# Kernel tuning notes

Measured on AMD Instinct MI355X. Metric: run time of the kernel, lower is better.

Reference implementation:

```python
import jax, jax.numpy as jnp
import numpy as np

BS, T, H = 4, 2048, 512
N_HEAD = 8
D_HEAD = H // N_HEAD  # 64


def setup_inputs() -> dict:
    key = jax.random.key(0)
    k1, k2, k3 = jax.random.split(key, 3)
    x = jax.random.normal(k1, (BS, T, H), dtype=jnp.float32)
    # torch Linear(hidden, (2*n_head+1)*d_head) -> store transposed for x @ W
    w_qkv = jax.random.normal(k2, (H, (2 * N_HEAD + 1) * D_HEAD), dtype=jnp.float32) * (H ** -0.5)
    w_out = jax.random.normal(k3, (D_HEAD, H), dtype=jnp.float32) * (D_HEAD ** -0.5)
    return {"x": x, "w_qkv": w_qkv, "w_out": w_out}


def reference(x, w_qkv, w_out):
    bs, t, h = x.shape
    n_head, d_head = N_HEAD, D_HEAD
    scale = d_head ** -0.5

    qkv = x @ w_qkv  # [bs, t, (2*n_head+1)*d_head]
    q, k, v = jnp.split(qkv, [n_head * d_head, 2 * n_head * d_head], axis=-1)
    q = q.reshape(bs, t, n_head, d_head)
    k = k.reshape(bs, t, n_head, d_head)
    # v stays [bs, t, d_head]: a single V shared across all heads

    # causal mask: -inf strictly above the diagonal
    mask = jnp.triu(jnp.full((t, t), -jnp.inf, dtype=x.dtype), 1)

    # scores: [bs, n_head, t_q, t_k]
    attn_score = jnp.einsum('bqhd,bkhd->bhqk', q, k) * scale + mask
    attn_prob = jax.nn.softmax(attn_score, axis=-1)

    # shared V broadcast over heads: [bs, n_head, t, d_head]
    attn_vec = jnp.einsum('bhqk,bkd->bhqd', attn_prob, v)
    m_attn_vec = jnp.mean(attn_vec, axis=1)  # mean over heads -> [bs, t, d_head]

    out = m_attn_vec @ w_out  # [bs, t, hidden]
    return out, attn_prob
```

## Files before the change

kernel.cpp:

```cpp
#include <hip/hip_runtime.h>

typedef unsigned short u16;
typedef __bf16 bf16x8 __attribute__((ext_vector_type(8)));
typedef float f32x4 __attribute__((ext_vector_type(4)));
static_assert(sizeof(bf16x8) == 16, "bf16x8 must be 16B");

#define MFMA(a, b, c) __builtin_amdgcn_mfma_f32_16x16x32_bf16(a, b, c, 0, 0, 0)

__device__ __forceinline__ u16 f2bf(float f) {
  unsigned u = __float_as_uint(f);
  u += 0x7fffu + ((u >> 16) & 1u);
  return (u16)(u >> 16);
}

__global__ __launch_bounds__(256) void prep_kernel(
    const float* __restrict__ x, const float* __restrict__ wqkv,
    const float* __restrict__ wout, u16* __restrict__ xh,
    u16* __restrict__ wt, u16* __restrict__ wot) {
  int blk = blockIdx.x, tid = threadIdx.x;
  if (blk < 4096) {
    int idx = (blk * 256 + tid) * 4;
    float4 v = *(const float4*)(x + idx);
    ushort4 o;
    o.x = f2bf(v.x); o.y = f2bf(v.y); o.z = f2bf(v.z); o.w = f2bf(v.w);
    *(ushort4*)(xh + idx) = o;
  } else if (blk < 4096 + 2176) {
    int idx = (blk - 4096) * 256 + tid;
    int n = idx >> 9, k = idx & 511;
    float v = wqkv[k * 1088 + n];
    if (n < 512) v *= 0.125f;
    wt[idx] = f2bf(v);
  } else {
    int idx = (blk - 6272) * 256 + tid;
    int n = idx >> 6, d = idx & 63;
    wot[idx] = f2bf(wout[d * 512 + n]);
  }
}

__global__ __launch_bounds__(256) void qkv_gemm_kernel(
    const u16* __restrict__ xh, const u16* __restrict__ wt,
    u16* __restrict__ Qb, u16* __restrict__ Kb, u16* __restrict__ Vt) {
  __shared__ u16 As[128][40];
  __shared__ u16 Bs[64][40];
  const int tid = threadIdx.x;
  const int w = tid >> 6, l = tid & 63, g = l >> 4, c16 = l & 15;
  const int n0 = blockIdx.x * 64;
  const int m0 = blockIdx.y * 128;
  const int arow = tid >> 1, acol = (tid & 1) << 4;
  const int brow = tid >> 2, bcol = (tid & 3) << 3;
  const u16* ap = xh + (size_t)(m0 + arow) * 512 + acol;
  const u16* bp = wt + (size_t)(n0 + brow) * 512 + bcol;
  uint4 pa0 = *(const uint4*)(ap);
  uint4 pa1 = *(const uint4*)(ap + 8);
  uint4 pb0 = *(const uint4*)(bp);
  f32x4 acc[2][4] = {};
  for (int k0 = 0; k0 < 512; k0 += 32) {
    __syncthreads();
    *(uint4*)&As[arow][acol] = pa0;
    *(uint4*)&As[arow][acol + 8] = pa1;
    *(uint4*)&Bs[brow][bcol] = pb0;
    __syncthreads();
    if (k0 + 32 < 512) {
      pa0 = *(const uint4*)(ap + k0 + 32);
      pa1 = *(const uint4*)(ap + k0 + 40);
      pb0 = *(const uint4*)(bp + k0 + 32);
    }
#pragma unroll
    for (int mt = 0; mt < 2; ++mt) {
      bf16x8 a = *(const bf16x8*)&As[w * 32 + mt * 16 + c16][g * 8];
#pragma unroll
      for (int nt = 0; nt < 4; ++nt) {
        bf16x8 b = *(const bf16x8*)&Bs[nt * 16 + c16][g * 8];
        acc[mt][nt] = MFMA(a, b, acc[mt][nt]);
      }
    }
  }
#pragma unroll
  for (int mt = 0; mt < 2; ++mt)
#pragma unroll
    for (int nt = 0; nt < 4; ++nt)
#pragma unroll
      for (int j = 0; j < 4; ++j) {
        u16 bv = f2bf(acc[mt][nt][j]);
        int row = m0 + w * 32 + mt * 16 + g * 4 + j;
        int b = row >> 11, t = row & 2047;
        int col = n0 + nt * 16 + c16;
        if (col < 512) {
          int h = col >> 6, d = col & 63;
          Qb[((size_t)((b << 3) + h) * 2048 + t) * 64 + d] = bv;
        } else if (col < 1024) {
          int cc = col - 512, h = cc >> 6, d = cc & 63;
          Kb[((size_t)((b << 3) + h) * 2048 + t) * 64 + d] = bv;
        } else {
          int d = col - 1024;
          Vt[((size_t)((b << 6) + d)) * 2048 + t] = bv;
        }
      }
}

__global__ __launch_bounds__(256) void attn_kernel(
    const u16* __restrict__ Qb, const u16* __restrict__ Kb,
    const u16* __restrict__ Vt, float* __restrict__ P,
    float* __restrict__ Obuf) {
  __shared__ u16 QP[64][72];
  __shared__ u16 Ks[64][72];
  __shared__ u16 Vs[64][72];
  const int tid = threadIdx.x;
  const int w = tid >> 6, l = tid & 63, g = l >> 4, c16 = l & 15;
  const int bidx = blockIdx.x;
  const int ii = bidx >> 5, jj = bidx & 31;
  const int qt = ((ii >> 3) & 1) ? (31 - jj) : jj;
  const int bh = ii, b = bh >> 3;
  const int srow = tid >> 2, scol = (tid & 3) << 4;

  {
    const u16* src = Qb + ((size_t)(bh * 2048 + qt * 64 + srow)) * 64 + scol;
    *(uint4*)&QP[srow][scol] = *(const uint4*)(src);
    *(uint4*)&QP[srow][scol + 8] = *(const uint4*)(src + 8);
  }
  __syncthreads();
  const bf16x8 aq0 = *(const bf16x8*)&QP[w * 16 + c16][g * 8];
  const bf16x8 aq1 = *(const bf16x8*)&QP[w * 16 + c16][32 + g * 8];

  const u16* kbase = Kb + ((size_t)bh * 2048) * 64;
  const u16* vbase = Vt + ((size_t)(b << 6)) * 2048;

  float lsum = 0.f;

  uint4 ka0 = *(const uint4*)(kbase + (size_t)srow * 64 + scol);
  uint4 ka1 = *(const uint4*)(kbase + (size_t)srow * 64 + scol + 8);
  for (int kt = 0; kt <= qt; ++kt) {
    __syncthreads();
    *(uint4*)&Ks[srow][scol] = ka0;
    *(uint4*)&Ks[srow][scol + 8] = ka1;
    __syncthreads();
    if (kt < qt) {
      const u16* knext = kbase + (size_t)((kt + 1) * 64 + srow) * 64 + scol;
      ka0 = *(const uint4*)(knext);
      ka1 = *(const uint4*)(knext + 8);
    }
    f32x4 st[4];
    __builtin_amdgcn_s_setprio(1);
#pragma unroll
    for (int nt = 0; nt < 4; ++nt) {
      bf16x8 k0 = *(const bf16x8*)&Ks[nt * 16 + c16][g * 8];
      bf16x8 k1 = *(const bf16x8*)&Ks[nt * 16 + c16][32 + g * 8];
      f32x4 a = {};
      a = MFMA(k0, aq0, a);
      a = MFMA(k1, aq1, a);
      st[nt] = a;
    }
    __builtin_amdgcn_s_setprio(0);
    if (kt == qt) {
#pragma unroll
      for (int nt = 0; nt < 4; ++nt)
#pragma unroll
        for (int j = 0; j < 4; ++j)
          if (nt * 16 + g * 4 + j > w * 16 + c16) st[nt][j] = -3.0e38f;
    }
#pragma unroll
    for (int nt = 0; nt < 4; ++nt)
#pragma unroll
      for (int j = 0; j < 4; ++j) lsum += __expf(st[nt][j]);
  }
  lsum += __shfl_xor(lsum, 16, 64);
  lsum += __shfl_xor(lsum, 32, 64);
  const float rl = 1.0f / lsum;

  f32x4 oacc[4] = {};
  ka0 = *(const uint4*)(kbase + (size_t)srow * 64 + scol);
  ka1 = *(const uint4*)(kbase + (size_t)srow * 64 + scol + 8);
  uint4 va0 = *(const uint4*)(vbase + (size_t)srow * 2048 + scol);
  uint4 va1 = *(const uint4*)(vbase + (size_t)srow * 2048 + scol + 8);
  float* prow = P +
      ((size_t)(bh * 2048 + qt * 64 + w * 16 + c16)) * 2048 + g * 4;
  for (int kt = 0; kt <= qt; ++kt) {
    __syncthreads();
    *(uint4*)&Ks[srow][scol] = ka0;
    *(uint4*)&Ks[srow][scol + 8] = ka1;
    *(uint4*)&Vs[srow][scol] = va0;
    *(uint4*)&Vs[srow][scol + 8] = va1;
    __syncthreads();
    if (kt < qt) {
      const u16* knext = kbase + (size_t)((kt + 1) * 64 + srow) * 64 + scol;
      ka0 = *(const uint4*)(knext);
      ka1 = *(const uint4*)(knext + 8);
      const u16* vnext = vbase + (size_t)srow * 2048 + (kt + 1) * 64 + scol;
      va0 = *(const uint4*)(vnext);
      va1 = *(const uint4*)(vnext + 8);
    }
    f32x4 st[4];
    __builtin_amdgcn_s_setprio(1);
#pragma unroll
    for (int nt = 0; nt < 4; ++nt) {
      bf16x8 k0 = *(const bf16x8*)&Ks[nt * 16 + c16][g * 8];
      bf16x8 k1 = *(const bf16x8*)&Ks[nt * 16 + c16][32 + g * 8];
      f32x4 a = {};
      a = MFMA(k0, aq0, a);
      a = MFMA(k1, aq1, a);
      st[nt] = a;
    }
    __builtin_amdgcn_s_setprio(0);
    if (kt == qt) {
#pragma unroll
      for (int nt = 0; nt < 4; ++nt)
#pragma unroll
        for (int j = 0; j < 4; ++j)
          if (nt * 16 + g * 4 + j > w * 16 + c16) st[nt][j] = -3.0e38f;
    }
#pragma unroll
    for (int nt = 0; nt < 4; ++nt) {
      f32x4 pv;
#pragma unroll
      for (int j = 0; j < 4; ++j) pv[j] = __expf(st[nt][j]) * rl;
      __builtin_nontemporal_store(
          pv, (f32x4*)(prow + (size_t)kt * 64 + nt * 16));
      unsigned r0, r1;
      asm("v_cvt_pk_bf16_f32 %0, %1, %2" : "=v"(r0) : "v"(pv[0]), "v"(pv[1]));
      asm("v_cvt_pk_bf16_f32 %0, %1, %2" : "=v"(r1) : "v"(pv[2]), "v"(pv[3]));
      uint2 pk; pk.x = r0; pk.y = r1;
      *(uint2*)&QP[w * 16 + c16][nt * 16 + g * 4] = pk;
    }
    bf16x8 ap0 = *(const bf16x8*)&QP[w * 16 + c16][g * 8];
    bf16x8 ap1 = *(const bf16x8*)&QP[w * 16 + c16][32 + g * 8];
    __builtin_amdgcn_s_setprio(1);
#pragma unroll
    for (int nt = 0; nt < 4; ++nt) {
      bf16x8 bv0 = *(const bf16x8*)&Vs[nt * 16 + c16][g * 8];
      bf16x8 bv1 = *(const bf16x8*)&Vs[nt * 16 + c16][32 + g * 8];
      oacc[nt] = MFMA(ap0, bv0, oacc[nt]);
      oacc[nt] = MFMA(ap1, bv1, oacc[nt]);
    }
    __builtin_amdgcn_s_setprio(0);
  }

  {
    float* obase = Obuf + ((size_t)(bh * 2048 + qt * 64 + w * 16)) * 64;
#pragma unroll
    for (int nt = 0; nt < 4; ++nt)
#pragma unroll
      for (int j = 0; j < 4; ++j)
        obase[(g * 4 + j) * 64 + nt * 16 + c16] = oacc[nt][j];
  }
  {
    int colstart = (qt + 1) * 64;
    int nf4 = (2048 - colstart) >> 2;
    float* base = P + ((size_t)(bh * 2048 + qt * 64)) * 2048;
    f32x4 z = {0.f, 0.f, 0.f, 0.f};
    for (int r = 0; r < 64; ++r) {
      f32x4* rowp = (f32x4*)(base + (size_t)r * 2048 + colstart);
      for (int u = tid; u < nf4; u += 256)
        __builtin_nontemporal_store(z, rowp + u);
    }
  }
}

__global__ __launch_bounds__(256) void mean_kernel(
    const float* __restrict__ Obuf, u16* __restrict__ meanb) {
  int o4 = blockIdx.x * 256 + threadIdx.x;
  int d4 = o4 & 15, t = (o4 >> 4) & 2047, b = o4 >> 15;
  f32x4 acc = {0.f, 0.f, 0.f, 0.f};
#pragma unroll
  for (int h = 0; h < 8; ++h) {
    f32x4 v = *(const f32x4*)(Obuf +
        ((size_t)((b << 3) + h) * 2048 + t) * 64 + d4 * 4);
    acc += v;
  }
  ushort4 o;
  o.x = f2bf(acc[0] * 0.125f); o.y = f2bf(acc[1] * 0.125f);
  o.z = f2bf(acc[2] * 0.125f); o.w = f2bf(acc[3] * 0.125f);
  *(ushort4*)(meanb + (size_t)o4 * 4) = o;
}

__global__ __launch_bounds__(256) void out_gemm_kernel(
    const u16* __restrict__ meanb, const u16* __restrict__ wot,
    float* __restrict__ out) {
  __shared__ u16 As[64][72];
  __shared__ u16 Bs[64][72];
  const int tid = threadIdx.x;
  const int w = tid >> 6, l = tid & 63, g = l >> 4, c16 = l & 15;
  const int n0 = blockIdx.x * 64;
  const int m0 = blockIdx.y * 64;
  const int srow = tid >> 2, scol = (tid & 3) << 4;
  {
    const u16* asrc = meanb + (size_t)(m0 + srow) * 64 + scol;
    *(uint4*)&As[srow][scol] = *(const uint4*)(asrc);
    *(uint4*)&As[srow][scol + 8] = *(const uint4*)(asrc + 8);
    const u16* bsrc = wot + (size_t)(n0 + srow) * 64 + scol;
    *(uint4*)&Bs[srow][scol] = *(const uint4*)(bsrc);
    *(uint4*)&Bs[srow][scol + 8] = *(const uint4*)(bsrc + 8);
  }
  __syncthreads();
  bf16x8 a0 = *(const bf16x8*)&As[w * 16 + c16][g * 8];
  bf16x8 a1 = *(const bf16x8*)&As[w * 16 + c16][32 + g * 8];
  f32x4 acc[4] = {};
#pragma unroll
  for (int nt = 0; nt < 4; ++nt) {
    bf16x8 b0 = *(const bf16x8*)&Bs[nt * 16 + c16][g * 8];
    bf16x8 b1 = *(const bf16x8*)&Bs[nt * 16 + c16][32 + g * 8];
    acc[nt] = MFMA(a0, b0, acc[nt]);
    acc[nt] = MFMA(a1, b1, acc[nt]);
  }
#pragma unroll
  for (int nt = 0; nt < 4; ++nt)
#pragma unroll
    for (int j = 0; j < 4; ++j)
      __builtin_nontemporal_store(
          acc[nt][j],
          out + (size_t)(m0 + w * 16 + g * 4 + j) * 512 + n0 + nt * 16 + c16);
}

extern "C" void kernel_launch(void* const* d_in, const int* in_sizes, int n_in,
                              void* d_out, int out_size, void* d_ws,
                              size_t ws_size, hipStream_t stream) {
  (void)in_sizes; (void)n_in; (void)out_size; (void)ws_size;
  const float* x = (const float*)d_in[0];
  const float* wqkv = (const float*)d_in[1];
  const float* wout = (const float*)d_in[2];
  float* out = (float*)d_out;
  float* P = out + 4194304;

  u16* xh = (u16*)d_ws;
  u16* wt = xh + 4194304;
  u16* wot = wt + 557056;
  u16* Qb = wot + 32768;
  u16* Kb = Qb + 4194304;
  u16* Vt = Kb + 4194304;
  float* Obuf = (float*)(Vt + 524288);
  u16* meanb = xh;

  hipLaunchKernelGGL(prep_kernel, dim3(6400), dim3(256), 0, stream,
                     x, wqkv, wout, xh, wt, wot);
  hipLaunchKernelGGL(qkv_gemm_kernel, dim3(17, 64), dim3(256), 0, stream,
                     xh, wt, Qb, Kb, Vt);
  hipLaunchKernelGGL(attn_kernel, dim3(1024), dim3(256), 0, stream,
                     Qb, Kb, Vt, P, Obuf);
  hipLaunchKernelGGL(mean_kernel, dim3(512), dim3(256), 0, stream,
                     Obuf, meanb);
  hipLaunchKernelGGL(out_gemm_kernel, dim3(8, 128), dim3(256), 0, stream,
                     meanb, wot, out);
}
```

Measured before the change: 665.6 us.

## Load K/V fragments directly from global memory, dropping LDS staging and barriers

The attention kernel no longer stages Q, K and V tiles through shared memory with double-buffered register prefetch and block-wide barriers. Each wave instead reads its MFMA operand fragments straight from global memory (relying on L1/L2 reuse across the four waves), and only a small LDS buffer is kept for the P tile. Launch bounds are raised to request higher occupancy. This removes barrier stalls and LDS traffic, but each K/V element is now fetched by all four waves and the explicit prefetch overlap is lost, so the loop depends on cache hits and latency hiding through occupancy.

```diff
diff --git a/kernel.cpp b/kernel.cpp
--- a/kernel.cpp
+++ b/kernel.cpp
@@ -98,53 +98,36 @@
       }
 }
 
-__global__ __launch_bounds__(256) void attn_kernel(
+__global__ __launch_bounds__(256, 4) void attn_kernel(
     const u16* __restrict__ Qb, const u16* __restrict__ Kb,
     const u16* __restrict__ Vt, float* __restrict__ P,
     float* __restrict__ Obuf) {
-  __shared__ u16 QP[64][72];
-  __shared__ u16 Ks[64][72];
-  __shared__ u16 Vs[64][72];
+  __shared__ u16 Ps[64][72];
   const int tid = threadIdx.x;
   const int w = tid >> 6, l = tid & 63, g = l >> 4, c16 = l & 15;
   const int bidx = blockIdx.x;
   const int ii = bidx >> 5, jj = bidx & 31;
   const int qt = ((ii >> 3) & 1) ? (31 - jj) : jj;
   const int bh = ii, b = bh >> 3;
-  const int srow = tid >> 2, scol = (tid & 3) << 4;
-
-  {
-    const u16* src = Qb + ((size_t)(bh * 2048 + qt * 64 + srow)) * 64 + scol;
-    *(uint4*)&QP[srow][scol] = *(const uint4*)(src);
-    *(uint4*)&QP[srow][scol + 8] = *(const uint4*)(src + 8);
-  }
-  __syncthreads();
-  const bf16x8 aq0 = *(const bf16x8*)&QP[w * 16 + c16][g * 8];
-  const bf16x8 aq1 = *(const bf16x8*)&QP[w * 16 + c16][32 + g * 8];
-
-  const u16* kbase = Kb + ((size_t)bh * 2048) * 64;
-  const u16* vbase = Vt + ((size_t)(b << 6)) * 2048;
+
+  const u16* qrow = Qb + ((size_t)(bh * 2048 + qt * 64 + w * 16 + c16)) * 64;
+  const bf16x8 aq0 = *(const bf16x8*)(qrow + g * 8);
+  const bf16x8 aq1 = *(const bf16x8*)(qrow + 32 + g * 8);
+
+  const u16* kb = Kb + ((size_t)bh * 2048) * 64;
+  const u16* vb = Vt + ((size_t)(b << 6)) * 2048;
 
   float lsum = 0.f;
 
-  uint4 ka0 = *(const uint4*)(kbase + (size_t)srow * 64 + scol);
-  uint4 ka1 = *(const uint4*)(kbase + (size_t)srow * 64 + scol + 8);
   for (int kt = 0; kt <= qt; ++kt) {
-    __syncthreads();
-    *(uint4*)&Ks[srow][scol] = ka0;
-    *(uint4*)&Ks[srow][scol + 8] = ka1;
-    __syncthreads();
-    if (kt < qt) {
-      const u16* knext = kbase + (size_t)((kt + 1) * 64 + srow) * 64 + scol;
-      ka0 = *(const uint4*)(knext);
-      ka1 = *(const uint4*)(knext + 8);
-    }
+    const u16* kp = kb + (size_t)kt * 4096;
     f32x4 st[4];
     __builtin_amdgcn_s_setprio(1);
 #pragma unroll
     for (int nt = 0; nt < 4; ++nt) {
-      bf16x8 k0 = *(const bf16x8*)&Ks[nt * 16 + c16][g * 8];
-      bf16x8 k1 = *(const bf16x8*)&Ks[nt * 16 + c16][32 + g * 8];
+      const u16* kr = kp + (size_t)(nt * 16 + c16) * 64 + g * 8;
+      bf16x8 k0 = *(const bf16x8*)(kr);
+      bf16x8 k1 = *(const bf16x8*)(kr + 32);
       f32x4 a = {};
       a = MFMA(k0, aq0, a);
       a = MFMA(k1, aq1, a);
@@ -168,33 +151,17 @@
   const float rl = 1.0f / lsum;
 
   f32x4 oacc[4] = {};
-  ka0 = *(const uint4*)(kbase + (size_t)srow * 64 + scol);
-  ka1 = *(const uint4*)(kbase + (size_t)srow * 64 + scol + 8);
-  uint4 va0 = *(const uint4*)(vbase + (size_t)srow * 2048 + scol);
-  uint4 va1 = *(const uint4*)(vbase + (size_t)srow * 2048 + scol + 8);
   float* prow = P +
       ((size_t)(bh * 2048 + qt * 64 + w * 16 + c16)) * 2048 + g * 4;
   for (int kt = 0; kt <= qt; ++kt) {
-    __syncthreads();
-    *(uint4*)&Ks[srow][scol] = ka0;
-    *(uint4*)&Ks[srow][scol + 8] = ka1;
-    *(uint4*)&Vs[srow][scol] = va0;
-    *(uint4*)&Vs[srow][scol + 8] = va1;
-    __syncthreads();
-    if (kt < qt) {
-      const u16* knext = kbase + (size_t)((kt + 1) * 64 + srow) * 64 + scol;
-      ka0 = *(const uint4*)(knext);
-      ka1 = *(const uint4*)(knext + 8);
-      const u16* vnext = vbase + (size_t)srow * 2048 + (kt + 1) * 64 + scol;
-      va0 = *(const uint4*)(vnext);
-      va1 = *(const uint4*)(vnext + 8);
-    }
+    const u16* kp = kb + (size_t)kt * 4096;
     f32x4 st[4];
     __builtin_amdgcn_s_setprio(1);
 #pragma unroll
     for (int nt = 0; nt < 4; ++nt) {
-      bf16x8 k0 = *(const bf16x8*)&Ks[nt * 16 + c16][g * 8];
-      bf16x8 k1 = *(const bf16x8*)&Ks[nt * 16 + c16][32 + g * 8];
+      const u16* kr = kp + (size_t)(nt * 16 + c16) * 64 + g * 8;
+      bf16x8 k0 = *(const bf16x8*)(kr);
+      bf16x8 k1 = *(const bf16x8*)(kr + 32);
       f32x4 a = {};
       a = MFMA(k0, aq0, a);
       a = MFMA(k1, aq1, a);
@@ -219,17 +186,18 @@
       asm("v_cvt_pk_bf16_f32 %0, %1, %2" : "=v"(r0) : "v"(pv[0]), "v"(pv[1]));
       asm("v_cvt_pk_bf16_f32 %0, %1, %2" : "=v"(r1) : "v"(pv[2]), "v"(pv[3]));
       uint2 pk; pk.x = r0; pk.y = r1;
-      *(uint2*)&QP[w * 16 + c16][nt * 16 + g * 4] = pk;
-    }
-    bf16x8 ap0 = *(const bf16x8*)&QP[w * 16 + c16][g * 8];
-    bf16x8 ap1 = *(const bf16x8*)&QP[w * 16 + c16][32 + g * 8];
+      *(uint2*)&Ps[w * 16 + c16][nt * 16 + g * 4] = pk;
+    }
+    bf16x8 ap0 = *(const bf16x8*)&Ps[w * 16 + c16][g * 8];
+    bf16x8 ap1 = *(const bf16x8*)&Ps[w * 16 + c16][32 + g * 8];
     __builtin_amdgcn_s_setprio(1);
 #pragma unroll
     for (int nt = 0; nt < 4; ++nt) {
-      bf16x8 bv0 = *(const bf16x8*)&Vs[nt * 16 + c16][g * 8];
-      bf16x8 bv1 = *(const bf16x8*)&Vs[nt * 16 + c16][32 + g * 8];
-      oacc[nt] = MFMA(ap0, bv0, oacc[nt]);
-      oacc[nt] = MFMA(ap1, bv1, oacc[nt]);
+      const u16* vr = vb + (size_t)(nt * 16 + c16) * 2048 + kt * 64 + g * 8;
+      bf16x8 v0 = *(const bf16x8*)(vr);
+      bf16x8 v1 = *(const bf16x8*)(vr + 32);
+      oacc[nt] = MFMA(ap0, v0, oacc[nt]);
+      oacc[nt] = MFMA(ap1, v1, oacc[nt]);
     }
     __builtin_amdgcn_s_setprio(0);
   }
```

Result: slower. 700.0 us (+5.2%).
